# Performance work log

Measured on AMD Instinct MI355X. Metric: run time of the kernel, lower is better.

Reference implementation:

```python
import jax, jax.numpy as jnp
import numpy as np

VOCAB, EMB, HIDDEN, OUT = 50000, 300, 512, 2
SEQ, BATCH = 512, 1024


def setup_inputs() -> dict:
    key = jax.random.key(0)
    k_text, k_len, k_emb, k_w1, k_b1, k_w2, k_b2 = jax.random.split(key, 7)
    text = jax.random.randint(k_text, (SEQ, BATCH), 1, VOCAB, dtype=jnp.int64 if jax.config.jax_enable_x64 else jnp.int32)
    lengths = jax.random.randint(k_len, (BATCH,), 1, SEQ + 1, dtype=text.dtype)
    emb_table = jax.random.normal(k_emb, (VOCAB, EMB), dtype=jnp.float32) * 0.1
    emb_table = emb_table.at[0].set(0.0)  # padding_idx=0 row zeroed like nn.Embedding
    W1 = jax.random.normal(k_w1, (EMB, HIDDEN), dtype=jnp.float32) * (1.0 / np.sqrt(EMB))
    b1 = jax.random.normal(k_b1, (HIDDEN,), dtype=jnp.float32) * 0.01
    W2 = jax.random.normal(k_w2, (HIDDEN, OUT), dtype=jnp.float32) * (1.0 / np.sqrt(HIDDEN))
    b2 = jax.random.normal(k_b2, (OUT,), dtype=jnp.float32) * 0.01
    return {"text": text, "lengths": lengths, "emb_table": emb_table,
            "W1": W1, "b1": b1, "W2": W2, "b2": b2}


def reference(text, lengths, emb_table, W1, b1, W2, b2):
    # text: [S, B] int; embedding lookup -> [S, B, E]
    embedded = emb_table[text]
    # masked mean over the first `lengths[b]` tokens (vectorized segment mean)
    seq = embedded.shape[0]
    mask = (jnp.arange(seq)[:, None] < lengths[None, :]).astype(embedded.dtype)  # [S, B]
    pooled = jnp.einsum('sbe,sb->be', embedded, mask) / lengths[:, None].astype(embedded.dtype)  # [B, E]
    # fc1 -> (dropout p=0, identity) -> relu -> fc2
    h = jax.nn.relu(pooled @ W1 + b1)
    return h @ W2 + b2
```

## Files before the change

kernel.cpp:

```cpp
#include <hip/hip_runtime.h>

constexpr int EMB    = 300;
constexpr int EMB4   = 75;
constexpr int HIDDEN = 512;
constexpr int SEQ    = 512;
constexpr int BATCH  = 1024;
constexpr int VOCAB  = 50000;
constexpr int NBUK   = 32;
constexpr int BDIV   = 1563;
constexpr int PB     = 4;
constexpr int GFC1   = 16;

__device__ __forceinline__ float4 f4add(float4 a, float4 b) {
    return make_float4(a.x + b.x, a.y + b.y, a.z + b.z, a.w + b.w);
}

__global__ __launch_bounds__(256) void bucketize_kernel(
    const int* __restrict__ text,
    const int* __restrict__ lengths,
    int* __restrict__ btok,
    int* __restrict__ boff)
{
    const int wave = threadIdx.x >> 6;
    const int lane = threadIdx.x & 63;
    const int b    = blockIdx.x * 4 + wave;
    const int len  = lengths[b];
    const unsigned long long ltmask = (1ull << lane) - 1ull;

    int cnt = 0;
#pragma unroll
    for (int c = 0; c < 8; ++c) {
        const int s = c * 64 + lane;
        int k = NBUK;
        if (s < len) k = text[(size_t)s * BATCH + b] / BDIV;
        for (int kk = 0; kk < NBUK; ++kk) {
            const unsigned long long m = __ballot(k == kk);
            if (lane == kk) cnt += __popcll(m);
        }
    }
    int incl = cnt;
#pragma unroll
    for (int off = 1; off < 32; off <<= 1) {
        const int v = __shfl_up(incl, off);
        if (lane >= off && lane < NBUK) incl += v;
    }
    const int excl = incl - cnt;
    if (lane < NBUK)  boff[b * (NBUK + 1) + lane] = excl;
    if (lane == NBUK - 1) boff[b * (NBUK + 1) + NBUK] = incl;

    int base = excl;
#pragma unroll
    for (int c = 0; c < 8; ++c) {
        const int s = c * 64 + lane;
        int tok = 0, k = NBUK;
        if (s < len) { tok = text[(size_t)s * BATCH + b]; k = tok / BDIV; }
        unsigned long long mym = 0;
        int chunkcnt = 0;
        for (int kk = 0; kk < NBUK; ++kk) {
            const unsigned long long m = __ballot(k == kk);
            if (k == kk) mym = m;
            if (lane == kk) chunkcnt = __popcll(m);
        }
        const int rank = __popcll(mym & ltmask);
        const int pos  = __shfl(base, k) + rank;
        if (s < len) btok[(size_t)b * SEQ + pos] = tok;
        base += chunkcnt;
    }
}

__global__ __launch_bounds__(320) void pool_kernel(
    const int* __restrict__ btok,
    const int* __restrict__ boff,
    const float* __restrict__ emb,
    float* __restrict__ partial,
    int NX)
{
    const int x  = blockIdx.x % NX;
    const int b0 = (blockIdx.x / NX) * PB;
    const int NJ = NBUK / NX;

    __shared__ int toks[PB][SEQ];
    __shared__ int seg[PB][2];

    if (threadIdx.x < PB) {
        const int b  = b0 + threadIdx.x;
        const int lo = boff[b * (NBUK + 1) + x * NJ];
        const int hi = boff[b * (NBUK + 1) + x * NJ + NJ];
        seg[threadIdx.x][0] = lo;
        seg[threadIdx.x][1] = hi - lo;
    }
    __syncthreads();

    for (int g = 0; g < PB; ++g) {
        const int lo = seg[g][0], n = seg[g][1];
        for (int t = threadIdx.x; t < n; t += 320)
            toks[g][t] = btok[(size_t)(b0 + g) * SEQ + lo + t];
    }
    __syncthreads();

    const int g = threadIdx.x / 80;
    const int c = threadIdx.x % 80;
    if (c < EMB4) {
        const int n = seg[g][1];
        float4 A = make_float4(0.f, 0.f, 0.f, 0.f);
        float4 B = A;
        int i = 0;
        for (; i + 8 <= n; i += 8) {
            const int t0 = toks[g][i + 0];
            const int t1 = toks[g][i + 1];
            const int t2 = toks[g][i + 2];
            const int t3 = toks[g][i + 3];
            const int t4 = toks[g][i + 4];
            const int t5 = toks[g][i + 5];
            const int t6 = toks[g][i + 6];
            const int t7 = toks[g][i + 7];
            const float4 v0 = ((const float4*)(emb + (size_t)t0 * EMB))[c];
            const float4 v1 = ((const float4*)(emb + (size_t)t1 * EMB))[c];
            const float4 v2 = ((const float4*)(emb + (size_t)t2 * EMB))[c];
            const float4 v3 = ((const float4*)(emb + (size_t)t3 * EMB))[c];
            const float4 v4 = ((const float4*)(emb + (size_t)t4 * EMB))[c];
            const float4 v5 = ((const float4*)(emb + (size_t)t5 * EMB))[c];
            const float4 v6 = ((const float4*)(emb + (size_t)t6 * EMB))[c];
            const float4 v7 = ((const float4*)(emb + (size_t)t7 * EMB))[c];
            A = f4add(A, f4add(f4add(v0, v1), f4add(v2, v3)));
            B = f4add(B, f4add(f4add(v4, v5), f4add(v6, v7)));
        }
        for (; i + 4 <= n; i += 4) {
            const float4 v0 = ((const float4*)(emb + (size_t)toks[g][i + 0] * EMB))[c];
            const float4 v1 = ((const float4*)(emb + (size_t)toks[g][i + 1] * EMB))[c];
            const float4 v2 = ((const float4*)(emb + (size_t)toks[g][i + 2] * EMB))[c];
            const float4 v3 = ((const float4*)(emb + (size_t)toks[g][i + 3] * EMB))[c];
            A = f4add(A, f4add(f4add(v0, v1), f4add(v2, v3)));
        }
        for (; i < n; ++i)
            B = f4add(B, ((const float4*)(emb + (size_t)toks[g][i] * EMB))[c]);
        A = f4add(A, B);
        ((float4*)(partial + ((size_t)x * BATCH + b0 + g) * EMB))[c] = A;
    }
}

template<int NX>
__global__ __launch_bounds__(512) void fc1_kernel(
    const float* __restrict__ partial,
    const int* __restrict__ lengths,
    const float* __restrict__ W1,
    const float* __restrict__ b1,
    float* __restrict__ hbuf)
{
    __shared__ float4 pQ[GFC1 / 4][EMB];
    const int b0  = blockIdx.x * GFC1;
    const int tid = threadIdx.x;

    float* pQf = (float*)pQ;
    for (int i = tid; i < EMB * GFC1; i += 512) {
        const int g = i / EMB;
        const int e = i - g * EMB;
        float s = 0.f;
#pragma unroll
        for (int xx = 0; xx < NX; ++xx)
            s += partial[((size_t)xx * BATCH + b0 + g) * EMB + e];
        pQf[((g >> 2) * EMB + e) * 4 + (g & 3)] = s / (float)lengths[b0 + g];
    }
    __syncthreads();

    const int j  = blockIdx.y * 128 + (tid & 127);
    const int gs = tid >> 7;
    const float bias = b1[j];
    float4 acc = make_float4(bias, bias, bias, bias);

    for (int e = 0; e < EMB; e += 10) {
        const float w0 = W1[(size_t)(e + 0) * HIDDEN + j];
        const float w1 = W1[(size_t)(e + 1) * HIDDEN + j];
        const float w2 = W1[(size_t)(e + 2) * HIDDEN + j];
        const float w3 = W1[(size_t)(e + 3) * HIDDEN + j];
        const float w4 = W1[(size_t)(e + 4) * HIDDEN + j];
        const float w5 = W1[(size_t)(e + 5) * HIDDEN + j];
        const float w6 = W1[(size_t)(e + 6) * HIDDEN + j];
        const float w7 = W1[(size_t)(e + 7) * HIDDEN + j];
        const float w8 = W1[(size_t)(e + 8) * HIDDEN + j];
        const float w9 = W1[(size_t)(e + 9) * HIDDEN + j];
        const float4 p0 = pQ[gs][e + 0];
        const float4 p1 = pQ[gs][e + 1];
        const float4 p2 = pQ[gs][e + 2];
        const float4 p3 = pQ[gs][e + 3];
        const float4 p4 = pQ[gs][e + 4];
        const float4 p5 = pQ[gs][e + 5];
        const float4 p6 = pQ[gs][e + 6];
        const float4 p7 = pQ[gs][e + 7];
        const float4 p8 = pQ[gs][e + 8];
        const float4 p9 = pQ[gs][e + 9];
        acc.x += p0.x * w0 + p1.x * w1 + p2.x * w2 + p3.x * w3 + p4.x * w4
               + p5.x * w5 + p6.x * w6 + p7.x * w7 + p8.x * w8 + p9.x * w9;
        acc.y += p0.y * w0 + p1.y * w1 + p2.y * w2 + p3.y * w3 + p4.y * w4
               + p5.y * w5 + p6.y * w6 + p7.y * w7 + p8.y * w8 + p9.y * w9;
        acc.z += p0.z * w0 + p1.z * w1 + p2.z * w2 + p3.z * w3 + p4.z * w4
               + p5.z * w5 + p6.z * w6 + p7.z * w7 + p8.z * w8 + p9.z * w9;
        acc.w += p0.w * w0 + p1.w * w1 + p2.w * w2 + p3.w * w3 + p4.w * w4
               + p5.w * w5 + p6.w * w6 + p7.w * w7 + p8.w * w8 + p9.w * w9;
    }
    const int bb = b0 + gs * 4;
    hbuf[(size_t)(bb + 0) * HIDDEN + j] = fmaxf(acc.x, 0.f);
    hbuf[(size_t)(bb + 1) * HIDDEN + j] = fmaxf(acc.y, 0.f);
    hbuf[(size_t)(bb + 2) * HIDDEN + j] = fmaxf(acc.z, 0.f);
    hbuf[(size_t)(bb + 3) * HIDDEN + j] = fmaxf(acc.w, 0.f);
}

__global__ __launch_bounds__(256) void fc2_kernel(
    const float* __restrict__ hbuf,
    const float* __restrict__ W2,
    const float* __restrict__ b2,
    float* __restrict__ out)
{
    const int wave = threadIdx.x >> 6;
    const int lane = threadIdx.x & 63;
    const int b    = blockIdx.x * 4 + wave;

    const float4* hrow = (const float4*)(hbuf + (size_t)b * HIDDEN);
    const float4* W2v  = (const float4*)W2;
    float s0 = 0.f, s1 = 0.f;
#pragma unroll
    for (int q = 0; q < 2; ++q) {
        const int c = lane + q * 64;
        const float4 h  = hrow[c];
        const float4 wA = W2v[2 * c + 0];
        const float4 wB = W2v[2 * c + 1];
        s0 += h.x * wA.x + h.y * wA.z + h.z * wB.x + h.w * wB.z;
        s1 += h.x * wA.y + h.y * wA.w + h.z * wB.y + h.w * wB.w;
    }
#pragma unroll
    for (int off = 32; off > 0; off >>= 1) {
        s0 += __shfl_down(s0, off);
        s1 += __shfl_down(s1, off);
    }
    if (lane == 0) {
        out[b * 2 + 0] = s0 + b2[0];
        out[b * 2 + 1] = s1 + b2[1];
    }
}

extern "C" void kernel_launch(void* const* d_in, const int* in_sizes, int n_in,
                              void* d_out, int out_size, void* d_ws, size_t ws_size,
                              hipStream_t stream) {
    const int*   text    = (const int*)d_in[0];
    const int*   lengths = (const int*)d_in[1];
    const float* emb     = (const float*)d_in[2];
    const float* W1      = (const float*)d_in[3];
    const float* b1      = (const float*)d_in[4];
    const float* W2      = (const float*)d_in[5];
    const float* b2      = (const float*)d_in[6];
    float*       out     = (float*)d_out;

    char* ws = (char*)d_ws;
    const size_t btokBytes = (size_t)BATCH * SEQ * sizeof(int);
    const size_t boffBytes = (size_t)BATCH * (NBUK + 1) * sizeof(int);
    const size_t poolBytes = (size_t)BATCH * EMB * sizeof(float);
    const size_t hbufBytes = (size_t)BATCH * HIDDEN * sizeof(float);

    int*   btok = (int*)ws;
    int*   boff = (int*)(ws + btokBytes);
    float* partial = (float*)(ws + btokBytes + boffBytes);

    const size_t fixed = btokBytes + boffBytes + hbufBytes;
    int NX = 1;
    if      (ws_size >= fixed + 8 * poolBytes) NX = 8;
    else if (ws_size >= fixed + 4 * poolBytes) NX = 4;
    else if (ws_size >= fixed + 2 * poolBytes) NX = 2;
    float* hbuf = (float*)(ws + btokBytes + boffBytes + (size_t)NX * poolBytes);

    bucketize_kernel<<<BATCH / 4, 256, 0, stream>>>(text, lengths, btok, boff);
    pool_kernel<<<NX * (BATCH / PB), 320, 0, stream>>>(btok, boff, emb, partial, NX);

    dim3 fgrid(BATCH / GFC1, HIDDEN / 128);
    switch (NX) {
        case 8: fc1_kernel<8><<<fgrid, 512, 0, stream>>>(partial, lengths, W1, b1, hbuf); break;
        case 4: fc1_kernel<4><<<fgrid, 512, 0, stream>>>(partial, lengths, W1, b1, hbuf); break;
        case 2: fc1_kernel<2><<<fgrid, 512, 0, stream>>>(partial, lengths, W1, b1, hbuf); break;
        default: fc1_kernel<1><<<fgrid, 512, 0, stream>>>(partial, lengths, W1, b1, hbuf); break;
    }
    fc2_kernel<<<BATCH / 4, 256, 0, stream>>>(hbuf, W2, b2, out);
}
```

Measured before the change: 72.91 us.

## Fuse fc1 and fc2, rewrite bucketize with bit-ballots, inline-asm gather loads

Bucketization now stages the text tile in shared memory and ranks tokens with 6 bit-ballots plus a shared histogram, replacing 32 ballots per chunk. The pooling loop issues eight gather loads in one inline-asm block with a single waitcnt. fc1 and fc2 are fused into one MLP kernel that keeps the hidden activations in LDS, which removes the hbuf round trip and one launch. In exchange, fc1 now has only 64 blocks covering all 512 hidden units each, so parallelism drops, and the inline asm limits how the compiler can schedule the loads.

```diff
diff --git a/kernel.cpp b/kernel.cpp
--- a/kernel.cpp
+++ b/kernel.cpp
@@ -1,19 +1,16 @@
 #include <hip/hip_runtime.h>
+
+typedef float f32x4 __attribute__((ext_vector_type(4)));
 
 constexpr int EMB    = 300;
 constexpr int EMB4   = 75;
 constexpr int HIDDEN = 512;
 constexpr int SEQ    = 512;
 constexpr int BATCH  = 1024;
-constexpr int VOCAB  = 50000;
 constexpr int NBUK   = 32;
 constexpr int BDIV   = 1563;
 constexpr int PB     = 4;
 constexpr int GFC1   = 16;
-
-__device__ __forceinline__ float4 f4add(float4 a, float4 b) {
-    return make_float4(a.x + b.x, a.y + b.y, a.z + b.z, a.w + b.w);
-}
 
 __global__ __launch_bounds__(256) void bucketize_kernel(
     const int* __restrict__ text,
@@ -21,51 +18,92 @@
     int* __restrict__ btok,
     int* __restrict__ boff)
 {
-    const int wave = threadIdx.x >> 6;
-    const int lane = threadIdx.x & 63;
-    const int b    = blockIdx.x * 4 + wave;
+    __shared__ int4 tstage[SEQ];
+    __shared__ int  hist[4][8][NBUK + 2];
+
+    const int tid  = threadIdx.x;
+    const int wave = tid >> 6;
+    const int lane = tid & 63;
+    const int b0   = blockIdx.x * 4;
+    const int b    = b0 + wave;
     const int len  = lengths[b];
-    const unsigned long long ltmask = (1ull << lane) - 1ull;
-
-    int cnt = 0;
+    const unsigned long long lt = (1ull << lane) - 1ull;
+
+    for (int s = tid; s < SEQ; s += 256)
+        tstage[s] = *(const int4*)&text[(size_t)s * BATCH + b0];
+    for (int i = tid; i < 4 * 8 * (NBUK + 2); i += 256)
+        ((int*)hist)[i] = 0;
+    __syncthreads();
+
+    int tokv[8], kv[8], rkv[8];
 #pragma unroll
     for (int c = 0; c < 8; ++c) {
-        const int s = c * 64 + lane;
-        int k = NBUK;
-        if (s < len) k = text[(size_t)s * BATCH + b] / BDIV;
-        for (int kk = 0; kk < NBUK; ++kk) {
-            const unsigned long long m = __ballot(k == kk);
-            if (lane == kk) cnt += __popcll(m);
-        }
-    }
-    int incl = cnt;
+        const int s      = c * 64 + lane;
+        const bool valid = s < len;
+        const int tok = valid ? ((const int*)&tstage[s])[wave] : 0;
+        const int k   = valid ? tok / BDIV : NBUK;
+        unsigned long long mm = ~0ull;
+#pragma unroll
+        for (int bit = 0; bit < 6; ++bit) {
+            const unsigned long long bl = __ballot((k >> bit) & 1);
+            mm &= ((k >> bit) & 1) ? bl : ~bl;
+        }
+        const int rk = __popcll(mm & lt);
+        tokv[c] = tok; kv[c] = k; rkv[c] = rk;
+        if (valid && rk == 0) hist[wave][c][k] = __popcll(mm);
+    }
+    __syncthreads();
+
+    int tot = 0;
+    if (lane < NBUK) {
+#pragma unroll
+        for (int c = 0; c < 8; ++c) {
+            const int t = hist[wave][c][lane];
+            hist[wave][c][lane] = tot;
+            tot += t;
+        }
+    }
+    int incl = tot;
 #pragma unroll
     for (int off = 1; off < 32; off <<= 1) {
         const int v = __shfl_up(incl, off);
         if (lane >= off && lane < NBUK) incl += v;
     }
-    const int excl = incl - cnt;
-    if (lane < NBUK)  boff[b * (NBUK + 1) + lane] = excl;
+    const int excl = incl - tot;
+    if (lane < NBUK)      boff[b * (NBUK + 1) + lane] = excl;
     if (lane == NBUK - 1) boff[b * (NBUK + 1) + NBUK] = incl;
-
-    int base = excl;
+    __syncthreads();
+
 #pragma unroll
     for (int c = 0; c < 8; ++c) {
-        const int s = c * 64 + lane;
-        int tok = 0, k = NBUK;
-        if (s < len) { tok = text[(size_t)s * BATCH + b]; k = tok / BDIV; }
-        unsigned long long mym = 0;
-        int chunkcnt = 0;
-        for (int kk = 0; kk < NBUK; ++kk) {
-            const unsigned long long m = __ballot(k == kk);
-            if (k == kk) mym = m;
-            if (lane == kk) chunkcnt = __popcll(m);
-        }
-        const int rank = __popcll(mym & ltmask);
-        const int pos  = __shfl(base, k) + rank;
-        if (s < len) btok[(size_t)b * SEQ + pos] = tok;
-        base += chunkcnt;
-    }
+        const int s  = c * 64 + lane;
+        const int k  = kv[c];
+        const int bb = __shfl(excl, k);
+        const int pos = bb + hist[wave][c][k] + rkv[c];
+        if (s < len) btok[(size_t)b * SEQ + pos] = tokv[c];
+    }
+}
+
+__device__ __forceinline__ void gather8(
+    const f32x4* a0, const f32x4* a1, const f32x4* a2, const f32x4* a3,
+    const f32x4* a4, const f32x4* a5, const f32x4* a6, const f32x4* a7,
+    f32x4& v0, f32x4& v1, f32x4& v2, f32x4& v3,
+    f32x4& v4, f32x4& v5, f32x4& v6, f32x4& v7)
+{
+    asm volatile(
+        "global_load_dwordx4 %0, %8, off\n\t"
+        "global_load_dwordx4 %1, %9, off\n\t"
+        "global_load_dwordx4 %2, %10, off\n\t"
+        "global_load_dwordx4 %3, %11, off\n\t"
+        "global_load_dwordx4 %4, %12, off\n\t"
+        "global_load_dwordx4 %5, %13, off\n\t"
+        "global_load_dwordx4 %6, %14, off\n\t"
+        "global_load_dwordx4 %7, %15, off\n\t"
+        "s_waitcnt vmcnt(0)"
+        : "=&v"(v0), "=&v"(v1), "=&v"(v2), "=&v"(v3),
+          "=&v"(v4), "=&v"(v5), "=&v"(v6), "=&v"(v7)
+        : "v"(a0), "v"(a1), "v"(a2), "v"(a3),
+          "v"(a4), "v"(a5), "v"(a6), "v"(a7));
 }
 
 __global__ __launch_bounds__(320) void pool_kernel(
@@ -102,52 +140,47 @@
     const int c = threadIdx.x % 80;
     if (c < EMB4) {
         const int n = seg[g][1];
-        float4 A = make_float4(0.f, 0.f, 0.f, 0.f);
-        float4 B = A;
+        const f32x4* e4 = (const f32x4*)emb;
+        f32x4 A = {0.f, 0.f, 0.f, 0.f};
+        f32x4 B = A;
         int i = 0;
         for (; i + 8 <= n; i += 8) {
-            const int t0 = toks[g][i + 0];
-            const int t1 = toks[g][i + 1];
-            const int t2 = toks[g][i + 2];
-            const int t3 = toks[g][i + 3];
-            const int t4 = toks[g][i + 4];
-            const int t5 = toks[g][i + 5];
-            const int t6 = toks[g][i + 6];
-            const int t7 = toks[g][i + 7];
-            const float4 v0 = ((const float4*)(emb + (size_t)t0 * EMB))[c];
-            const float4 v1 = ((const float4*)(emb + (size_t)t1 * EMB))[c];
-            const float4 v2 = ((const float4*)(emb + (size_t)t2 * EMB))[c];
-            const float4 v3 = ((const float4*)(emb + (size_t)t3 * EMB))[c];
-            const float4 v4 = ((const float4*)(emb + (size_t)t4 * EMB))[c];
-            const float4 v5 = ((const float4*)(emb + (size_t)t5 * EMB))[c];
-            const float4 v6 = ((const float4*)(emb + (size_t)t6 * EMB))[c];
-            const float4 v7 = ((const float4*)(emb + (size_t)t7 * EMB))[c];
-            A = f4add(A, f4add(f4add(v0, v1), f4add(v2, v3)));
-            B = f4add(B, f4add(f4add(v4, v5), f4add(v6, v7)));
-        }
-        for (; i + 4 <= n; i += 4) {
-            const float4 v0 = ((const float4*)(emb + (size_t)toks[g][i + 0] * EMB))[c];
-            const float4 v1 = ((const float4*)(emb + (size_t)toks[g][i + 1] * EMB))[c];
-            const float4 v2 = ((const float4*)(emb + (size_t)toks[g][i + 2] * EMB))[c];
-            const float4 v3 = ((const float4*)(emb + (size_t)toks[g][i + 3] * EMB))[c];
-            A = f4add(A, f4add(f4add(v0, v1), f4add(v2, v3)));
+            const int4 ta = *(const int4*)&toks[g][i];
+            const int4 tb = *(const int4*)&toks[g][i + 4];
+            const f32x4* a0 = e4 + (size_t)ta.x * EMB4 + c;
+            const f32x4* a1 = e4 + (size_t)ta.y * EMB4 + c;
+            const f32x4* a2 = e4 + (size_t)ta.z * EMB4 + c;
+            const f32x4* a3 = e4 + (size_t)ta.w * EMB4 + c;
+            const f32x4* a4 = e4 + (size_t)tb.x * EMB4 + c;
+            const f32x4* a5 = e4 + (size_t)tb.y * EMB4 + c;
+            const f32x4* a6 = e4 + (size_t)tb.z * EMB4 + c;
+            const f32x4* a7 = e4 + (size_t)tb.w * EMB4 + c;
+            f32x4 v0, v1, v2, v3, v4, v5, v6, v7;
+            gather8(a0, a1, a2, a3, a4, a5, a6, a7,
+                    v0, v1, v2, v3, v4, v5, v6, v7);
+            A += (v0 + v1) + (v2 + v3);
+            B += (v4 + v5) + (v6 + v7);
         }
         for (; i < n; ++i)
-            B = f4add(B, ((const float4*)(emb + (size_t)toks[g][i] * EMB))[c]);
-        A = f4add(A, B);
-        ((float4*)(partial + ((size_t)x * BATCH + b0 + g) * EMB))[c] = A;
+            A += e4[(size_t)toks[g][i] * EMB4 + c];
+        A += B;
+        ((f32x4*)(partial + ((size_t)x * BATCH + b0 + g) * EMB))[c] = A;
     }
 }
 
 template<int NX>
-__global__ __launch_bounds__(512) void fc1_kernel(
+__global__ __launch_bounds__(512) void mlp_kernel(
     const float* __restrict__ partial,
     const int* __restrict__ lengths,
     const float* __restrict__ W1,
     const float* __restrict__ b1,
-    float* __restrict__ hbuf)
-{
-    __shared__ float4 pQ[GFC1 / 4][EMB];
+    const float* __restrict__ W2,
+    const float* __restrict__ b2,
+    float* __restrict__ out)
+{
+    __shared__ f32x4 pQ[GFC1 / 4][EMB];
+    __shared__ float hsh[GFC1][HIDDEN];
+
     const int b0  = blockIdx.x * GFC1;
     const int tid = threadIdx.x;
 
@@ -163,78 +196,52 @@
     }
     __syncthreads();
 
-    const int j  = blockIdx.y * 128 + (tid & 127);
-    const int gs = tid >> 7;
+    const int j = tid;
     const float bias = b1[j];
-    float4 acc = make_float4(bias, bias, bias, bias);
-
-    for (int e = 0; e < EMB; e += 10) {
-        const float w0 = W1[(size_t)(e + 0) * HIDDEN + j];
-        const float w1 = W1[(size_t)(e + 1) * HIDDEN + j];
-        const float w2 = W1[(size_t)(e + 2) * HIDDEN + j];
-        const float w3 = W1[(size_t)(e + 3) * HIDDEN + j];
-        const float w4 = W1[(size_t)(e + 4) * HIDDEN + j];
-        const float w5 = W1[(size_t)(e + 5) * HIDDEN + j];
-        const float w6 = W1[(size_t)(e + 6) * HIDDEN + j];
-        const float w7 = W1[(size_t)(e + 7) * HIDDEN + j];
-        const float w8 = W1[(size_t)(e + 8) * HIDDEN + j];
-        const float w9 = W1[(size_t)(e + 9) * HIDDEN + j];
-        const float4 p0 = pQ[gs][e + 0];
-        const float4 p1 = pQ[gs][e + 1];
-        const float4 p2 = pQ[gs][e + 2];
-        const float4 p3 = pQ[gs][e + 3];
-        const float4 p4 = pQ[gs][e + 4];
-        const float4 p5 = pQ[gs][e + 5];
-        const float4 p6 = pQ[gs][e + 6];
-        const float4 p7 = pQ[gs][e + 7];
-        const float4 p8 = pQ[gs][e + 8];
-        const float4 p9 = pQ[gs][e + 9];
-        acc.x += p0.x * w0 + p1.x * w1 + p2.x * w2 + p3.x * w3 + p4.x * w4
-               + p5.x * w5 + p6.x * w6 + p7.x * w7 + p8.x * w8 + p9.x * w9;
-        acc.y += p0.y * w0 + p1.y * w1 + p2.y * w2 + p3.y * w3 + p4.y * w4
-               + p5.y * w5 + p6.y * w6 + p7.y * w7 + p8.y * w8 + p9.y * w9;
-        acc.z += p0.z * w0 + p1.z * w1 + p2.z * w2 + p3.z * w3 + p4.z * w4
-               + p5.z * w5 + p6.z * w6 + p7.z * w7 + p8.z * w8 + p9.z * w9;
-        acc.w += p0.w * w0 + p1.w * w1 + p2.w * w2 + p3.w * w3 + p4.w * w4
-               + p5.w * w5 + p6.w * w6 + p7.w * w7 + p8.w * w8 + p9.w * w9;
-    }
-    const int bb = b0 + gs * 4;
-    hbuf[(size_t)(bb + 0) * HIDDEN + j] = fmaxf(acc.x, 0.f);
-    hbuf[(size_t)(bb + 1) * HIDDEN + j] = fmaxf(acc.y, 0.f);
-    hbuf[(size_t)(bb + 2) * HIDDEN + j] = fmaxf(acc.z, 0.f);
-    hbuf[(size_t)(bb + 3) * HIDDEN + j] = fmaxf(acc.w, 0.f);
-}
-
-__global__ __launch_bounds__(256) void fc2_kernel(
-    const float* __restrict__ hbuf,
-    const float* __restrict__ W2,
-    const float* __restrict__ b2,
-    float* __restrict__ out)
-{
-    const int wave = threadIdx.x >> 6;
-    const int lane = threadIdx.x & 63;
-    const int b    = blockIdx.x * 4 + wave;
-
-    const float4* hrow = (const float4*)(hbuf + (size_t)b * HIDDEN);
-    const float4* W2v  = (const float4*)W2;
-    float s0 = 0.f, s1 = 0.f;
-#pragma unroll
-    for (int q = 0; q < 2; ++q) {
-        const int c = lane + q * 64;
-        const float4 h  = hrow[c];
-        const float4 wA = W2v[2 * c + 0];
-        const float4 wB = W2v[2 * c + 1];
-        s0 += h.x * wA.x + h.y * wA.z + h.z * wB.x + h.w * wB.z;
-        s1 += h.x * wA.y + h.y * wA.w + h.z * wB.y + h.w * wB.w;
-    }
-#pragma unroll
-    for (int off = 32; off > 0; off >>= 1) {
-        s0 += __shfl_down(s0, off);
-        s1 += __shfl_down(s1, off);
-    }
-    if (lane == 0) {
-        out[b * 2 + 0] = s0 + b2[0];
-        out[b * 2 + 1] = s1 + b2[1];
+    f32x4 acc[4];
+#pragma unroll
+    for (int q = 0; q < 4; ++q) acc[q] = (f32x4){bias, bias, bias, bias};
+
+#pragma unroll 5
+    for (int e = 0; e < EMB; ++e) {
+        const float w = W1[(size_t)e * HIDDEN + j];
+#pragma unroll
+        for (int q = 0; q < 4; ++q) acc[q] += pQ[q][e] * w;
+    }
+#pragma unroll
+    for (int q = 0; q < 4; ++q) {
+        hsh[q * 4 + 0][j] = fmaxf(acc[q].x, 0.f);
+        hsh[q * 4 + 1][j] = fmaxf(acc[q].y, 0.f);
+        hsh[q * 4 + 2][j] = fmaxf(acc[q].z, 0.f);
+        hsh[q * 4 + 3][j] = fmaxf(acc[q].w, 0.f);
+    }
+    __syncthreads();
+
+    const int w    = tid >> 6;
+    const int lane = tid & 63;
+    const f32x4* W2v = (const f32x4*)W2;
+#pragma unroll
+    for (int rr = 0; rr < 2; ++rr) {
+        const int r = w * 2 + rr;
+        float s0 = 0.f, s1 = 0.f;
+#pragma unroll
+        for (int q = 0; q < 2; ++q) {
+            const int cc = lane + q * 64;
+            const f32x4 hv = *(const f32x4*)&hsh[r][4 * cc];
+            const f32x4 wA = W2v[2 * cc + 0];
+            const f32x4 wB = W2v[2 * cc + 1];
+            s0 += hv.x * wA.x + hv.y * wA.z + hv.z * wB.x + hv.w * wB.z;
+            s1 += hv.x * wA.y + hv.y * wA.w + hv.z * wB.y + hv.w * wB.w;
+        }
+#pragma unroll
+        for (int off = 32; off > 0; off >>= 1) {
+            s0 += __shfl_down(s0, off);
+            s1 += __shfl_down(s1, off);
+        }
+        if (lane == 0) {
+            out[(b0 + r) * 2 + 0] = s0 + b2[0];
+            out[(b0 + r) * 2 + 1] = s1 + b2[1];
+        }
     }
 }
 
@@ -254,28 +261,24 @@
     const size_t btokBytes = (size_t)BATCH * SEQ * sizeof(int);
     const size_t boffBytes = (size_t)BATCH * (NBUK + 1) * sizeof(int);
     const size_t poolBytes = (size_t)BATCH * EMB * sizeof(float);
-    const size_t hbufBytes = (size_t)BATCH * HIDDEN * sizeof(float);
-
-    int*   btok = (int*)ws;
-    int*   boff = (int*)(ws + btokBytes);
+
+    int*   btok    = (int*)ws;
+    int*   boff    = (int*)(ws + btokBytes);
     float* partial = (float*)(ws + btokBytes + boffBytes);
 
-    const size_t fixed = btokBytes + boffBytes + hbufBytes;
+    const size_t fixed = btokBytes + boffBytes;
     int NX = 1;
     if      (ws_size >= fixed + 8 * poolBytes) NX = 8;
     else if (ws_size >= fixed + 4 * poolBytes) NX = 4;
     else if (ws_size >= fixed + 2 * poolBytes) NX = 2;
-    float* hbuf = (float*)(ws + btokBytes + boffBytes + (size_t)NX * poolBytes);
 
     bucketize_kernel<<<BATCH / 4, 256, 0, stream>>>(text, lengths, btok, boff);
     pool_kernel<<<NX * (BATCH / PB), 320, 0, stream>>>(btok, boff, emb, partial, NX);
 
-    dim3 fgrid(BATCH / GFC1, HIDDEN / 128);
     switch (NX) {
-        case 8: fc1_kernel<8><<<fgrid, 512, 0, stream>>>(partial, lengths, W1, b1, hbuf); break;
-        case 4: fc1_kernel<4><<<fgrid, 512, 0, stream>>>(partial, lengths, W1, b1, hbuf); break;
-        case 2: fc1_kernel<2><<<fgrid, 512, 0, stream>>>(partial, lengths, W1, b1, hbuf); break;
-        default: fc1_kernel<1><<<fgrid, 512, 0, stream>>>(partial, lengths, W1, b1, hbuf); break;
-    }
-    fc2_kernel<<<BATCH / 4, 256, 0, stream>>>(hbuf, W2, b2, out);
-}
+        case 8:  mlp_kernel<8><<<BATCH / GFC1, 512, 0, stream>>>(partial, lengths, W1, b1, W2, b2, out); break;
+        case 4:  mlp_kernel<4><<<BATCH / GFC1, 512, 0, stream>>>(partial, lengths, W1, b1, W2, b2, out); break;
+        case 2:  mlp_kernel<2><<<BATCH / GFC1, 512, 0, stream>>>(partial, lengths, W1, b1, W2, b2, out); break;
+        default: mlp_kernel<1><<<BATCH / GFC1, 512, 0, stream>>>(partial, lengths, W1, b1, W2, b2, out); break;
+    }
+}
```

Measured after the change: 75.07 us. +3.0%, slower.
